# Kernel tuning notes

Measured on AMD Instinct MI355X. Metric: run time of the kernel, lower is better.

## Reference

```python
import jax, jax.numpy as jnp
import numpy as np

DIM = 256
HEADS = 8
HEAD_DIM = DIM // HEADS
SCALE = HEAD_DIM ** -0.5
B, N = 2048, 49
NW = 64


def setup_inputs() -> dict:
    key = jax.random.key(0)
    ks = jax.random.split(key, 7)
    x = jax.random.normal(ks[0], (B, N, DIM), dtype=jnp.float32)
    mask = jax.random.normal(ks[1], (NW, N + 1, N + 1), dtype=jnp.float32)
    class_token = 0.02 * jax.random.normal(ks[2], (1, 1, DIM), dtype=jnp.float32)
    qkv_w = jax.random.normal(ks[3], (DIM, 3 * DIM), dtype=jnp.float32) / np.sqrt(DIM)
    qkv_b = jnp.zeros((3 * DIM,), dtype=jnp.float32)
    proj_w = jax.random.normal(ks[4], (DIM, DIM), dtype=jnp.float32) / np.sqrt(DIM)
    proj_b = jnp.zeros((DIM,), dtype=jnp.float32)
    return {"x": x, "mask": mask, "class_token": class_token,
            "qkv_w": qkv_w, "qkv_b": qkv_b, "proj_w": proj_w, "proj_b": proj_b}


def reference(x, mask, class_token, qkv_w, qkv_b, proj_w, proj_b):
    b, n, c = x.shape
    n1 = n + 1
    # prepend learnable class token
    cls = jnp.broadcast_to(class_token, (b, 1, c))
    xc = jnp.concatenate([cls, x], axis=1)  # (B, N+1, C)
    # fused qkv projection
    qkv = xc @ qkv_w + qkv_b                 # (B, N+1, 3C)
    qkv = qkv.reshape(b, n1, 3, HEADS, HEAD_DIM)
    qkv = jnp.transpose(qkv, (2, 0, 3, 1, 4))  # (3, B, H, N+1, Dh)
    q, k, v = qkv[0] * SCALE, qkv[1], qkv[2]
    attn = jnp.einsum('bhid,bhjd->bhij', q, k)  # (B, H, N+1, N+1)
    # per-window additive mask bias
    nw = mask.shape[0]
    attn = attn.reshape(b // nw, nw, HEADS, n1, n1) + mask[None, :, None]
    attn = attn.reshape(b, HEADS, n1, n1)
    attn = jax.nn.softmax(attn, axis=-1)
    out = jnp.einsum('bhij,bhjd->bhid', attn, v)      # (B, H, N+1, Dh)
    out = jnp.transpose(out, (0, 2, 1, 3)).reshape(b, n1, c)
    out = out @ proj_w + proj_b
    return out[:, 0], out[:, 1:]
```

## Files before the change

kernel.cpp:

```cpp
#include <hip/hip_runtime.h>

#define NB    2048
#define N1    50
#define DIMC  256
#define NHEAD 8

typedef short  s16x8 __attribute__((ext_vector_type(8)));
typedef short  s16x4 __attribute__((ext_vector_type(4)));
typedef float  f32x4 __attribute__((ext_vector_type(4)));
typedef float  f32x2 __attribute__((ext_vector_type(2)));
typedef unsigned int u32x2 __attribute__((ext_vector_type(2)));

__device__ __forceinline__ unsigned short f2bf(float f) {
    unsigned int u = __builtin_bit_cast(unsigned int, f);
    u = (u + 0x7FFFu + ((u >> 16) & 1u)) >> 16;
    return (unsigned short)u;
}
__device__ __forceinline__ s16x8 ld8(const unsigned short* p) {
    return *(const s16x8*)p;
}

__global__ void prep_kernel(const float* __restrict__ qkv_w, const float* __restrict__ proj_w,
                            const float* __restrict__ mask,
                            unsigned short* __restrict__ wqkvB, unsigned short* __restrict__ wprojB,
                            float* __restrict__ maskP) {
    int idx = blockIdx.x * 256 + threadIdx.x;
    {
        int wv = idx >> 12, q = (idx >> 6) & 63, k = idx & 63;
        float v = (k < 50) ? ((q < 50) ? mask[(wv * 50 + q) * 50 + k] : 0.f) : -1e30f;
        maskP[idx] = v;
    }
    if (idx < 196608) {
        int ks = idx / 24576, rem = idx - ks * 24576, n = rem >> 5, kk = rem & 31;
        wqkvB[idx] = f2bf(qkv_w[(ks * 32 + kk) * 768 + n]);
    }
    if (idx < 65536) {
        int ks = idx >> 13, rem = idx & 8191, n = rem >> 5, kk = rem & 31;
        wprojB[idx] = f2bf(proj_w[(ks * 32 + kk) * 256 + n]);
    }
}

__global__ __launch_bounds__(1024, 4) void fused_kernel(
        const float* __restrict__ x, const float* __restrict__ cls,
        const float* __restrict__ qkv_b, const unsigned short* __restrict__ wqkvB,
        const unsigned short* __restrict__ wprojB, const float* __restrict__ proj_b,
        const float* __restrict__ maskP, float* __restrict__ out) {
    __shared__ __align__(16) char smem_raw[152576];
    unsigned short* S   = (unsigned short*)smem_raw;
    unsigned short* sXC = S;
    unsigned short* sQ  = S + 16896;
    unsigned short* sK  = S + 37376;
    unsigned short* sVT = S + 57856;

    const int b = blockIdx.x, tid = threadIdx.x;
    const int lane = tid & 63, w = tid >> 6;
    const int ln15 = lane & 15, quad = lane >> 4, q8 = quad * 8;
    const int win = b & 63;
    const float SCALE = 0.17677669529663687f;

    #pragma unroll
    for (int it = 0; it < 4; ++it) {
        const int r = it * 16 + w;
        f32x4 t;
        if (r == 0)       t = *(const f32x4*)&cls[lane * 4];
        else if (r <= 49) t = *(const f32x4*)&x[((size_t)b * 49 + (r - 1)) * 256 + lane * 4];
        else              t = f32x4{0.f, 0.f, 0.f, 0.f};
        u32x2 wv;
        wv[0] = (unsigned int)f2bf(t[0]) | ((unsigned int)f2bf(t[1]) << 16);
        wv[1] = (unsigned int)f2bf(t[2]) | ((unsigned int)f2bf(t[3]) << 16);
        *(u32x2*)&sXC[r * 264 + lane * 4] = wv;
    }
    s16x8 bcur[3];
    #pragma unroll
    for (int nt = 0; nt < 3; ++nt)
        bcur[nt] = ld8(wqkvB + (nt * 256 + w * 16 + ln15) * 32 + q8);
    __syncthreads();

    f32x4 acc[4][3];
    #pragma unroll
    for (int mt = 0; mt < 4; ++mt)
        #pragma unroll
        for (int nt = 0; nt < 3; ++nt) acc[mt][nt] = f32x4{0.f, 0.f, 0.f, 0.f};

    #pragma unroll
    for (int ks = 0; ks < 8; ++ks) {
        s16x8 bnext[3];
        if (ks < 7) {
            const unsigned short* src = wqkvB + (ks + 1) * 24576;
            #pragma unroll
            for (int nt = 0; nt < 3; ++nt)
                bnext[nt] = ld8(src + (nt * 256 + w * 16 + ln15) * 32 + q8);
        }
        s16x8 af[4];
        #pragma unroll
        for (int mt = 0; mt < 4; ++mt)
            af[mt] = ld8(&sXC[(mt * 16 + ln15) * 264 + ks * 32 + q8]);
        #pragma unroll
        for (int mt = 0; mt < 4; ++mt) {
            acc[mt][0] = __builtin_amdgcn_mfma_f32_16x16x32_bf16(bcur[0], af[mt], acc[mt][0], 0, 0, 0);
            acc[mt][1] = __builtin_amdgcn_mfma_f32_16x16x32_bf16(bcur[1], af[mt], acc[mt][1], 0, 0, 0);
            acc[mt][2] = __builtin_amdgcn_mfma_f32_16x16x32_bf16(af[mt], bcur[2], acc[mt][2], 0, 0, 0);
        }
        if (ks < 7) {
            #pragma unroll
            for (int nt = 0; nt < 3; ++nt) bcur[nt] = bnext[nt];
        }
    }

    {
        const int hd = w >> 1, ddb = (w & 1) * 16;
        const f32x4 bq4 = *(const f32x4*)&qkv_b[w * 16 + quad * 4];
        const f32x4 bk4 = *(const f32x4*)&qkv_b[256 + w * 16 + quad * 4];
        const float bv  = qkv_b[512 + w * 16 + ln15];
        #pragma unroll
        for (int mt = 0; mt < 4; ++mt) {
            const int row = (mt * 16 + ln15) * 40 + ddb + quad * 4;
            s16x4 wq, wk, wv;
            #pragma unroll
            for (int i = 0; i < 4; ++i) {
                wq[i] = f2bf((acc[mt][0][i] + bq4[i]) * SCALE);
                wk[i] = f2bf(acc[mt][1][i] + bk4[i]);
                wv[i] = f2bf(acc[mt][2][i] + bv);
            }
            *(s16x4*)&sQ[hd * 2560 + row] = wq;
            *(s16x4*)&sK[hd * 2560 + row] = wk;
            *(s16x4*)&sVT[hd * 2304 + (ddb + ln15) * 72 + mt * 16 + quad * 4] = wv;
        }
    }
    __syncthreads();

    {
        const int h = w >> 1, rh = w & 1, qt0 = rh * 2;
        unsigned short* sPw = sQ + h * 2560 + rh * 1280;

        s16x8 ak[4];
        #pragma unroll
        for (int kt = 0; kt < 4; ++kt)
            ak[kt] = ld8(&sK[h * 2560 + (kt * 16 + ln15) * 40 + q8]);

        f32x4 st[2][4];
        #pragma unroll
        for (int mt = 0; mt < 2; ++mt) {
            s16x8 bq = ld8(&sQ[h * 2560 + ((qt0 + mt) * 16 + ln15) * 40 + q8]);
            #pragma unroll
            for (int kt = 0; kt < 4; ++kt) {
                f32x4 z = {0.f, 0.f, 0.f, 0.f};
                st[mt][kt] = __builtin_amdgcn_mfma_f32_16x16x32_bf16(ak[kt], bq, z, 0, 0, 0);
            }
        }
        s16x8 pb[2][2];
        #pragma unroll
        for (int mt = 0; mt < 2; ++mt) {
            float sum = 0.f;
            #pragma unroll
            for (int kt = 0; kt < 4; ++kt) {
                f32x4 mk = *(const f32x4*)&maskP[((size_t)(win * 64 + (qt0 + mt) * 16 + ln15)) * 64 + kt * 16 + quad * 4];
                #pragma unroll
                for (int i = 0; i < 4; ++i) {
                    float e = __expf(st[mt][kt][i] + mk[i]);
                    st[mt][kt][i] = e;
                    sum += e;
                }
            }
            sum += __shfl_xor(sum, 16, 64);
            sum += __shfl_xor(sum, 32, 64);
            const float inv = 1.f / sum;
            #pragma unroll
            for (int kt = 0; kt < 4; ++kt) {
                s16x4 pk;
                #pragma unroll
                for (int i = 0; i < 4; ++i) pk[i] = f2bf(st[mt][kt][i] * inv);
                *(s16x4*)&sPw[ln15 * 72 + kt * 16 + quad * 4] = pk;
            }
            asm volatile("s_waitcnt lgkmcnt(0)" ::: "memory");
            pb[mt][0] = ld8(&sPw[ln15 * 72 + q8]);
            pb[mt][1] = ld8(&sPw[ln15 * 72 + 32 + q8]);
        }
        s16x8 av[2][2];
        #pragma unroll
        for (int dt = 0; dt < 2; ++dt)
            #pragma unroll
            for (int kk = 0; kk < 2; ++kk)
                av[dt][kk] = ld8(&sVT[h * 2304 + (dt * 16 + ln15) * 72 + kk * 32 + q8]);
        f32x4 o[2][2];
        #pragma unroll
        for (int mt = 0; mt < 2; ++mt)
            #pragma unroll
            for (int dt = 0; dt < 2; ++dt) o[mt][dt] = f32x4{0.f, 0.f, 0.f, 0.f};
        #pragma unroll
        for (int mt = 0; mt < 2; ++mt)
            #pragma unroll
            for (int dt = 0; dt < 2; ++dt)
                #pragma unroll
                for (int kk = 0; kk < 2; ++kk)
                    o[mt][dt] = __builtin_amdgcn_mfma_f32_16x16x32_bf16(av[dt][kk], pb[mt][kk], o[mt][dt], 0, 0, 0);
        #pragma unroll
        for (int mt = 0; mt < 2; ++mt) {
            const int qg = (qt0 + mt) * 16 + ln15;
            #pragma unroll
            for (int dt = 0; dt < 2; ++dt) {
                s16x4 ov;
                #pragma unroll
                for (int i = 0; i < 4; ++i) ov[i] = f2bf(o[mt][dt][i]);
                *(s16x4*)&sXC[qg * 264 + h * 32 + dt * 16 + quad * 4] = ov;
            }
        }
    }
    const int wm3 = w >> 3, wn3 = w & 7;
    s16x8 b3[2];
    #pragma unroll
    for (int nt = 0; nt < 2; ++nt)
        b3[nt] = ld8(wprojB + (wn3 * 32 + nt * 16 + ln15) * 32 + q8);
    __syncthreads();

    {
        f32x4 a3[2][2];
        #pragma unroll
        for (int mt = 0; mt < 2; ++mt)
            #pragma unroll
            for (int nt = 0; nt < 2; ++nt) a3[mt][nt] = f32x4{0.f, 0.f, 0.f, 0.f};
        #pragma unroll
        for (int ks = 0; ks < 8; ++ks) {
            s16x8 b3n[2];
            if (ks < 7) {
                const unsigned short* src = wprojB + (ks + 1) * 8192;
                #pragma unroll
                for (int nt = 0; nt < 2; ++nt)
                    b3n[nt] = ld8(src + (wn3 * 32 + nt * 16 + ln15) * 32 + q8);
            }
            s16x8 af3[2];
            #pragma unroll
            for (int mt = 0; mt < 2; ++mt)
                af3[mt] = ld8(&sXC[(wm3 * 32 + mt * 16 + ln15) * 264 + ks * 32 + q8]);
            #pragma unroll
            for (int mt = 0; mt < 2; ++mt)
                #pragma unroll
                for (int nt = 0; nt < 2; ++nt)
                    a3[mt][nt] = __builtin_amdgcn_mfma_f32_16x16x32_bf16(b3[nt], af3[mt], a3[mt][nt], 0, 0, 0);
            if (ks < 7) {
                #pragma unroll
                for (int nt = 0; nt < 2; ++nt) b3[nt] = b3n[nt];
            }
        }
        #pragma unroll
        for (int nt = 0; nt < 2; ++nt) {
            const int cb = wn3 * 32 + nt * 16 + quad * 4;
            const f32x4 b4 = *(const f32x4*)&proj_b[cb];
            #pragma unroll
            for (int mt = 0; mt < 2; ++mt) {
                const int t = wm3 * 32 + mt * 16 + ln15;
                f32x4 v;
                #pragma unroll
                for (int i = 0; i < 4; ++i) v[i] = a3[mt][nt][i] + b4[i];
                if (t == 0)      *(f32x4*)&out[(size_t)b * 256 + cb] = v;
                else if (t < 50) *(f32x4*)&out[524288 + ((size_t)b * 49 + (t - 1)) * 256 + cb] = v;
            }
        }
    }
}

extern "C" void kernel_launch(void* const* d_in, const int* in_sizes, int n_in,
                              void* d_out, int out_size, void* d_ws, size_t ws_size,
                              hipStream_t stream) {
    const float* x      = (const float*)d_in[0];
    const float* mask   = (const float*)d_in[1];
    const float* cls    = (const float*)d_in[2];
    const float* qkv_w  = (const float*)d_in[3];
    const float* qkv_b  = (const float*)d_in[4];
    const float* proj_w = (const float*)d_in[5];
    const float* proj_b = (const float*)d_in[6];
    float* out = (float*)d_out;

    unsigned short* wqkvB  = (unsigned short*)d_ws;
    unsigned short* wprojB = (unsigned short*)((char*)d_ws + 393216);
    float*          maskP  = (float*)((char*)d_ws + 524288);

    prep_kernel<<<1024, 256, 0, stream>>>(qkv_w, proj_w, mask, wqkvB, wprojB, maskP);
    fused_kernel<<<NB, 1024, 0, stream>>>(x, cls, qkv_b, wqkvB, wprojB, proj_b, maskP, out);
}
```

Before: 303.9 us.

## Transpose softmax probabilities via shuffles, prefetch mask, and raise MFMA wave priority

```diff
diff --git a/kernel.cpp b/kernel.cpp
--- a/kernel.cpp
+++ b/kernel.cpp
@@ -10,11 +10,15 @@
 typedef float  f32x4 __attribute__((ext_vector_type(4)));
 typedef float  f32x2 __attribute__((ext_vector_type(2)));
 typedef unsigned int u32x2 __attribute__((ext_vector_type(2)));
+typedef unsigned int u32x4 __attribute__((ext_vector_type(4)));
 
 __device__ __forceinline__ unsigned short f2bf(float f) {
     unsigned int u = __builtin_bit_cast(unsigned int, f);
     u = (u + 0x7FFFu + ((u >> 16) & 1u)) >> 16;
     return (unsigned short)u;
+}
+__device__ __forceinline__ unsigned int pk2(float a, float b) {
+    return (unsigned int)f2bf(a) | ((unsigned int)f2bf(b) << 16);
 }
 __device__ __forceinline__ s16x8 ld8(const unsigned short* p) {
     return *(const s16x8*)p;
@@ -57,6 +61,7 @@
     const int ln15 = lane & 15, quad = lane >> 4, q8 = quad * 8;
     const int win = b & 63;
     const float SCALE = 0.17677669529663687f;
+    const int h = w >> 1, rh = w & 1, qt0 = rh * 2;
 
     #pragma unroll
     for (int it = 0; it < 4; ++it) {
@@ -66,8 +71,8 @@
         else if (r <= 49) t = *(const f32x4*)&x[((size_t)b * 49 + (r - 1)) * 256 + lane * 4];
         else              t = f32x4{0.f, 0.f, 0.f, 0.f};
         u32x2 wv;
-        wv[0] = (unsigned int)f2bf(t[0]) | ((unsigned int)f2bf(t[1]) << 16);
-        wv[1] = (unsigned int)f2bf(t[2]) | ((unsigned int)f2bf(t[3]) << 16);
+        wv[0] = pk2(t[0], t[1]);
+        wv[1] = pk2(t[2], t[3]);
         *(u32x2*)&sXC[r * 264 + lane * 4] = wv;
     }
     s16x8 bcur[3];
@@ -95,12 +100,14 @@
         #pragma unroll
         for (int mt = 0; mt < 4; ++mt)
             af[mt] = ld8(&sXC[(mt * 16 + ln15) * 264 + ks * 32 + q8]);
+        __builtin_amdgcn_s_setprio(1);
         #pragma unroll
         for (int mt = 0; mt < 4; ++mt) {
             acc[mt][0] = __builtin_amdgcn_mfma_f32_16x16x32_bf16(bcur[0], af[mt], acc[mt][0], 0, 0, 0);
             acc[mt][1] = __builtin_amdgcn_mfma_f32_16x16x32_bf16(bcur[1], af[mt], acc[mt][1], 0, 0, 0);
             acc[mt][2] = __builtin_amdgcn_mfma_f32_16x16x32_bf16(af[mt], bcur[2], acc[mt][2], 0, 0, 0);
         }
+        __builtin_amdgcn_s_setprio(0);
         if (ks < 7) {
             #pragma unroll
             for (int nt = 0; nt < 3; ++nt) bcur[nt] = bnext[nt];
@@ -127,12 +134,15 @@
             *(s16x4*)&sVT[hd * 2304 + (ddb + ln15) * 72 + mt * 16 + quad * 4] = wv;
         }
     }
+    f32x4 mk[2][4];
+    #pragma unroll
+    for (int mt = 0; mt < 2; ++mt)
+        #pragma unroll
+        for (int kt = 0; kt < 4; ++kt)
+            mk[mt][kt] = *(const f32x4*)&maskP[((size_t)(win * 64 + (qt0 + mt) * 16 + ln15)) * 64 + kt * 16 + quad * 4];
     __syncthreads();
 
     {
-        const int h = w >> 1, rh = w & 1, qt0 = rh * 2;
-        unsigned short* sPw = sQ + h * 2560 + rh * 1280;
-
         s16x8 ak[4];
         #pragma unroll
         for (int kt = 0; kt < 4; ++kt)
@@ -142,11 +152,13 @@
         #pragma unroll
         for (int mt = 0; mt < 2; ++mt) {
             s16x8 bq = ld8(&sQ[h * 2560 + ((qt0 + mt) * 16 + ln15) * 40 + q8]);
+            __builtin_amdgcn_s_setprio(1);
             #pragma unroll
             for (int kt = 0; kt < 4; ++kt) {
                 f32x4 z = {0.f, 0.f, 0.f, 0.f};
                 st[mt][kt] = __builtin_amdgcn_mfma_f32_16x16x32_bf16(ak[kt], bq, z, 0, 0, 0);
             }
+            __builtin_amdgcn_s_setprio(0);
         }
         s16x8 pb[2][2];
         #pragma unroll
@@ -154,10 +166,9 @@
             float sum = 0.f;
             #pragma unroll
             for (int kt = 0; kt < 4; ++kt) {
-                f32x4 mk = *(const f32x4*)&maskP[((size_t)(win * 64 + (qt0 + mt) * 16 + ln15)) * 64 + kt * 16 + quad * 4];
                 #pragma unroll
                 for (int i = 0; i < 4; ++i) {
-                    float e = __expf(st[mt][kt][i] + mk[i]);
+                    float e = __expf(st[mt][kt][i] + mk[mt][kt][i]);
                     st[mt][kt][i] = e;
                     sum += e;
                 }
@@ -165,16 +176,24 @@
             sum += __shfl_xor(sum, 16, 64);
             sum += __shfl_xor(sum, 32, 64);
             const float inv = 1.f / sum;
+            unsigned int wd[8];
             #pragma unroll
             for (int kt = 0; kt < 4; ++kt) {
-                s16x4 pk;
-                #pragma unroll
-                for (int i = 0; i < 4; ++i) pk[i] = f2bf(st[mt][kt][i] * inv);
-                *(s16x4*)&sPw[ln15 * 72 + kt * 16 + quad * 4] = pk;
-            }
-            asm volatile("s_waitcnt lgkmcnt(0)" ::: "memory");
-            pb[mt][0] = ld8(&sPw[ln15 * 72 + q8]);
-            pb[mt][1] = ld8(&sPw[ln15 * 72 + 32 + q8]);
+                wd[kt * 2]     = pk2(st[mt][kt][0] * inv, st[mt][kt][1] * inv);
+                wd[kt * 2 + 1] = pk2(st[mt][kt][2] * inv, st[mt][kt][3] * inv);
+            }
+            #pragma unroll
+            for (int kk = 0; kk < 2; ++kk) {
+                u32x4 t;
+                #pragma unroll
+                for (int j = 0; j < 4; ++j) {
+                    const int sl = ln15 + ((lane & 16) << 1) + ((j >> 1) << 4);
+                    unsigned int a = (unsigned int)__shfl((int)wd[4 * kk + (j & 1)], sl, 64);
+                    unsigned int c = (unsigned int)__shfl((int)wd[4 * kk + 2 + (j & 1)], sl, 64);
+                    t[j] = (lane & 32) ? c : a;
+                }
+                pb[mt][kk] = __builtin_bit_cast(s16x8, t);
+            }
         }
         s16x8 av[2][2];
         #pragma unroll
@@ -187,6 +206,7 @@
         for (int mt = 0; mt < 2; ++mt)
             #pragma unroll
             for (int dt = 0; dt < 2; ++dt) o[mt][dt] = f32x4{0.f, 0.f, 0.f, 0.f};
+        __builtin_amdgcn_s_setprio(1);
         #pragma unroll
         for (int mt = 0; mt < 2; ++mt)
             #pragma unroll
@@ -194,6 +214,7 @@
                 #pragma unroll
                 for (int kk = 0; kk < 2; ++kk)
                     o[mt][dt] = __builtin_amdgcn_mfma_f32_16x16x32_bf16(av[dt][kk], pb[mt][kk], o[mt][dt], 0, 0, 0);
+        __builtin_amdgcn_s_setprio(0);
         #pragma unroll
         for (int mt = 0; mt < 2; ++mt) {
             const int qg = (qt0 + mt) * 16 + ln15;
@@ -232,11 +253,13 @@
             #pragma unroll
             for (int mt = 0; mt < 2; ++mt)
                 af3[mt] = ld8(&sXC[(wm3 * 32 + mt * 16 + ln15) * 264 + ks * 32 + q8]);
+            __builtin_amdgcn_s_setprio(1);
             #pragma unroll
             for (int mt = 0; mt < 2; ++mt)
                 #pragma unroll
                 for (int nt = 0; nt < 2; ++nt)
                     a3[mt][nt] = __builtin_amdgcn_mfma_f32_16x16x32_bf16(b3[nt], af3[mt], a3[mt][nt], 0, 0, 0);
+            __builtin_amdgcn_s_setprio(0);
             if (ks < 7) {
                 #pragma unroll
                 for (int nt = 0; nt < 2; ++nt) b3[nt] = b3n[nt];
```

New measurement: 309.4 us. No clear change (+1.8%).
